# Kernel optimization log

Hardware: AMD Instinct MI355X
Metric: run time of the kernel (lower is better)

Reference implementation:

```python
import jax, jax.numpy as jnp
import numpy as np

B = 1024          # number of graphs
H = 8             # heads
EPS = 1e-5        # LayerNorm eps (torch default)
MEAN_RES_SCALE = 0.2


def _ln(x, w, b):
    mu = x.mean(-1, keepdims=True)
    var = ((x - mu) ** 2).mean(-1, keepdims=True)
    return (x - mu) / jnp.sqrt(var + EPS) * w + b


def setup_inputs() -> dict:
    key = jax.random.key(0)
    ks = jax.random.split(key, 10)
    N, D = 262144, 256
    s = 1.0 / np.sqrt(D)
    return {
        "h": jax.random.normal(ks[0], (N, D), jnp.float32),
        "batch": jnp.sort(jax.random.randint(ks[1], (N,), 0, B)),
        "cdr_mask": jax.random.bernoulli(ks[2], 0.2, (N,)),
        "iface_mask": jax.random.bernoulli(ks[3], 0.2, (N,)),
        "ln_kv_w": jnp.ones((D,), jnp.float32),
        "ln_kv_b": jnp.zeros((D,), jnp.float32),
        "ln_q_w": jnp.ones((D,), jnp.float32),
        "ln_q_b": jnp.zeros((D,), jnp.float32),
        "Wk": jax.random.normal(ks[4], (D, D), jnp.float32) * s,
        "Wv": jax.random.normal(ks[5], (D, D), jnp.float32) * s,
        "Wq": jax.random.normal(ks[6], (D, 2 * D), jnp.float32) * (1.0 / np.sqrt(2 * D)),
        "Wres": jax.random.normal(ks[7], (D, D), jnp.float32) * s,
        "Wout": jax.random.normal(ks[8], (D, D), jnp.float32) * s,
        "cdr_bias": jnp.asarray(0.6, jnp.float32),
        "iface_bias": jnp.asarray(0.8, jnp.float32),
        "logit_scale": jnp.asarray(1.0, jnp.float32),
    }


def reference(h, batch, cdr_mask, iface_mask, ln_kv_w, ln_kv_b, ln_q_w, ln_q_b,
              Wk, Wv, Wq, Wres, Wout, cdr_bias, iface_bias, logit_scale):
    N, D = h.shape
    hd = D // H
    # per-graph mean / max pooling (segment reductions; all segments non-empty)
    counts = jax.ops.segment_sum(jnp.ones((N,), h.dtype), batch, num_segments=B)[:, None]
    mean_raw = jax.ops.segment_sum(h, batch, num_segments=B) / counts      # [B,D]
    max_raw = jax.ops.segment_max(h, batch, num_segments=B)                # [B,D]
    # single query per graph (dropout = identity in eval)
    q = jnp.concatenate([mean_raw, max_raw], axis=-1) @ Wq.T               # [B,D]
    q = _ln(q, ln_q_w, ln_q_b).reshape(B, H, hd)                           # [B,H,hd]
    # keys / values per node
    h_ln = _ln(h, ln_kv_w, ln_kv_b)
    k = (h_ln @ Wk.T).reshape(N, H, hd)
    v = (h_ln @ Wv.T).reshape(N, H, hd)
    # attention logits with mask biases
    logit = (k * q[batch]).sum(-1) * (logit_scale / np.sqrt(hd))           # [N,H]
    logit = logit + cdr_bias * cdr_mask.astype(h.dtype)[:, None]
    logit = logit + iface_bias * iface_mask.astype(h.dtype)[:, None]
    # segment softmax over nodes of each graph
    m = jax.ops.segment_max(logit, batch, num_segments=B)                  # [B,H]
    e = jnp.exp(logit - m[batch])
    z = jax.ops.segment_sum(e, batch, num_segments=B)                      # [B,H]
    attn = e / z[batch]                                                    # [N,H]
    g = jax.ops.segment_sum(attn[..., None] * v, batch, num_segments=B)    # [B,H,hd]
    g = g.reshape(B, D)
    return g @ Wout.T + MEAN_RES_SCALE * (mean_raw @ Wres.T)               # [B,D]
```

## Files before the change

kernel.cpp:

```cpp
#include <hip/hip_runtime.h>

__global__ void k_offsets(const int* __restrict__ batch, int* __restrict__ start,
                          int N, int B) {
    int i = blockIdx.x * blockDim.x + threadIdx.x;
    if (i >= N) return;
    int b = batch[i];
    if (i == 0) {
        for (int g = 0; g <= b; ++g) start[g] = 0;
    } else {
        int pb = batch[i - 1];
        for (int g = pb + 1; g <= b; ++g) start[g] = i;
    }
    if (i == N - 1) {
        for (int g = b + 1; g <= B; ++g) start[g] = N;
    }
}

__global__ __launch_bounds__(256) void k_pool_q(
    const float* __restrict__ h, const int* __restrict__ start,
    const float* __restrict__ Wq, const float* __restrict__ Wk,
    const float* __restrict__ ln_q_w, const float* __restrict__ ln_q_b,
    const float* __restrict__ logit_scale,
    float* __restrict__ mean_raw, float* __restrict__ w_eff)
{
    const int g = blockIdx.x;
    const int d = threadIdx.x;
    const int s = start[g], e = start[g + 1];

    float sum = 0.f, mx = -INFINITY;
    int n = s;
    for (; n + 4 <= e; n += 4) {
        float a0 = h[(size_t)(n + 0) * 256 + d];
        float a1 = h[(size_t)(n + 1) * 256 + d];
        float a2 = h[(size_t)(n + 2) * 256 + d];
        float a3 = h[(size_t)(n + 3) * 256 + d];
        sum += (a0 + a1) + (a2 + a3);
        mx = fmaxf(mx, fmaxf(fmaxf(a0, a1), fmaxf(a2, a3)));
    }
    for (; n < e; ++n) {
        float a = h[(size_t)n * 256 + d];
        sum += a; mx = fmaxf(mx, a);
    }
    const float mean = sum / (float)(e - s);
    mean_raw[(size_t)g * 256 + d] = mean;

    __shared__ float X[512];
    __shared__ float QL[256];
    __shared__ float rs[4], rq[4];
    X[d] = mean;
    X[256 + d] = mx;
    __syncthreads();

    float q = 0.f;
    const float* wqr = Wq + (size_t)d * 512;
    #pragma unroll 8
    for (int j = 0; j < 512; j += 4) {
        float4 w4 = *(const float4*)(wqr + j);
        q += w4.x * X[j] + w4.y * X[j + 1] + w4.z * X[j + 2] + w4.w * X[j + 3];
    }
    float s1 = q, s2 = q * q;
    #pragma unroll
    for (int off = 1; off < 64; off <<= 1) {
        s1 += __shfl_xor(s1, off);
        s2 += __shfl_xor(s2, off);
    }
    if ((d & 63) == 0) { rs[d >> 6] = s1; rq[d >> 6] = s2; }
    __syncthreads();
    const float t1 = rs[0] + rs[1] + rs[2] + rs[3];
    const float t2 = rq[0] + rq[1] + rq[2] + rq[3];
    const float mu = t1 * (1.f / 256.f);
    const float var = t2 * (1.f / 256.f) - mu * mu;
    const float rstd = rsqrtf(var + 1e-5f);
    QL[d] = (q - mu) * rstd * ln_q_w[d] + ln_q_b[d];
    __syncthreads();

    const float scale = logit_scale[0] * 0.17677669529663687f;
    #pragma unroll
    for (int hh = 0; hh < 8; ++hh) {
        float a = 0.f;
        #pragma unroll 8
        for (int r = 0; r < 32; ++r) {
            a += Wk[(size_t)(hh * 32 + r) * 256 + d] * QL[hh * 32 + r];
        }
        w_eff[((size_t)g * 8 + hh) * 256 + d] = a * scale;
    }
}

__global__ __launch_bounds__(256) void k_attn(
    const float* __restrict__ h, const int* __restrict__ start,
    const int* __restrict__ cdr, const int* __restrict__ ifm,
    const float* __restrict__ ln_w, const float* __restrict__ ln_b,
    const float* __restrict__ w_eff,
    const float* __restrict__ cdr_bias, const float* __restrict__ iface_bias,
    float* __restrict__ u_norm)
{
    const int g = blockIdx.x;
    const int tid = threadIdx.x;
    const int w = tid >> 6;
    const int l = tid & 63;
    const int hh = l >> 3;
    const int p = l & 7;
    const int s = start[g], e = start[g + 1];
    const float cb = cdr_bias[0], ib = iface_bias[0];

    const float4 lnw = *(const float4*)(ln_w + l * 4);
    const float4 lnb = *(const float4*)(ln_b + l * 4);

    float we[32];
    {
        const float* wp = w_eff + ((size_t)g * 8 + hh) * 256 + p * 32;
        #pragma unroll
        for (int r = 0; r < 8; ++r) {
            float4 t = *(const float4*)(wp + r * 4);
            we[4 * r + 0] = t.x; we[4 * r + 1] = t.y; we[4 * r + 2] = t.z; we[4 * r + 3] = t.w;
        }
    }

    float m = -INFINITY, z = 0.f;
    float u[32];
    #pragma unroll
    for (int r = 0; r < 32; ++r) u[r] = 0.f;

    __shared__ float hbuf[4][288];
    __shared__ float UF[4][8][256];
    __shared__ float MW[4][8], ZW[4][8], FG[4][8], IZ[8];

    const int wofs = l * 4 + ((l >> 3) << 2);
    const int rofs = p * 36;

    for (int n = s + w; n < e; n += 4) {
        const float4 x = *(const float4*)(h + (size_t)n * 256 + l * 4);
        float s1 = (x.x + x.y) + (x.z + x.w);
        float s2 = x.x * x.x + x.y * x.y + x.z * x.z + x.w * x.w;
        #pragma unroll
        for (int off = 1; off < 64; off <<= 1) {
            s1 += __shfl_xor(s1, off);
            s2 += __shfl_xor(s2, off);
        }
        const float mu = s1 * (1.f / 256.f);
        const float var = s2 * (1.f / 256.f) - mu * mu;
        const float rstd = rsqrtf(var + 1e-5f);
        float4 hl;
        hl.x = (x.x - mu) * rstd * lnw.x + lnb.x;
        hl.y = (x.y - mu) * rstd * lnw.y + lnb.y;
        hl.z = (x.z - mu) * rstd * lnw.z + lnb.z;
        hl.w = (x.w - mu) * rstd * lnw.w + lnb.w;
        *(float4*)(&hbuf[w][wofs]) = hl;
        asm volatile("s_waitcnt lgkmcnt(0)" ::: "memory");

        float hv[32];
        #pragma unroll
        for (int r = 0; r < 8; ++r) {
            float4 t = *(const float4*)(&hbuf[w][rofs + r * 4]);
            hv[4 * r + 0] = t.x; hv[4 * r + 1] = t.y; hv[4 * r + 2] = t.z; hv[4 * r + 3] = t.w;
        }
        float part = 0.f;
        #pragma unroll
        for (int r = 0; r < 32; ++r) part += hv[r] * we[r];
        part += __shfl_xor(part, 1);
        part += __shfl_xor(part, 2);
        part += __shfl_xor(part, 4);

        const float mb = cb * (float)cdr[n] + ib * (float)ifm[n];
        const float lv = part + mb;
        const float nm = fmaxf(m, lv);
        const float a  = __expf(m - nm);
        const float ee = __expf(lv - nm);
        z = z * a + ee;
        #pragma unroll
        for (int r = 0; r < 32; ++r) u[r] = u[r] * a + ee * hv[r];
        m = nm;
    }

    if (p == 0) { MW[w][hh] = m; ZW[w][hh] = z; }
    #pragma unroll
    for (int r = 0; r < 8; ++r) {
        float4 t = make_float4(u[4 * r], u[4 * r + 1], u[4 * r + 2], u[4 * r + 3]);
        *(float4*)(&UF[w][hh][p * 32 + r * 4]) = t;
    }
    __syncthreads();

    if (tid < 8) {
        const float mg = fmaxf(fmaxf(MW[0][tid], MW[1][tid]),
                               fmaxf(MW[2][tid], MW[3][tid]));
        float zg = 0.f;
        #pragma unroll
        for (int ww = 0; ww < 4; ++ww) {
            const float f = __expf(MW[ww][tid] - mg);
            FG[ww][tid] = f;
            zg += ZW[ww][tid] * f;
        }
        IZ[tid] = 1.f / zg;
    }
    __syncthreads();

    #pragma unroll
    for (int it = 0; it < 8; ++it) {
        const int idx = it * 256 + tid;
        const int h2 = idx >> 8, j = idx & 255;
        const float v = UF[0][h2][j] * FG[0][h2] + UF[1][h2][j] * FG[1][h2]
                      + UF[2][h2][j] * FG[2][h2] + UF[3][h2][j] * FG[3][h2];
        u_norm[(size_t)g * 2048 + idx] = v * IZ[h2];
    }
}

__global__ __launch_bounds__(256) void k_out(
    const float* __restrict__ u_norm, const float* __restrict__ mean_raw,
    const float* __restrict__ Wv, const float* __restrict__ Wout,
    const float* __restrict__ Wres, float* __restrict__ out)
{
    const int d = threadIdx.x;
    const int g0 = blockIdx.x * 4;
    __shared__ float UN[4][8][256];
    __shared__ float MR[4][256];
    __shared__ float GF[4][256];

    for (int idx = d; idx < 4 * 2048; idx += 256)
        ((float*)UN)[idx] = u_norm[(size_t)g0 * 2048 + idx];
    for (int idx = d; idx < 4 * 256; idx += 256)
        ((float*)MR)[idx] = mean_raw[(size_t)g0 * 256 + idx];
    __syncthreads();

    const int hh = d >> 5;
    float acc[4] = {0.f, 0.f, 0.f, 0.f};
    const float* wvr = Wv + (size_t)d * 256;
    for (int j = 0; j < 256; j += 4) {
        const float4 wv = *(const float4*)(wvr + j);
        #pragma unroll
        for (int gg = 0; gg < 4; ++gg) {
            acc[gg] += wv.x * UN[gg][hh][j]     + wv.y * UN[gg][hh][j + 1]
                     + wv.z * UN[gg][hh][j + 2] + wv.w * UN[gg][hh][j + 3];
        }
    }
    #pragma unroll
    for (int gg = 0; gg < 4; ++gg) GF[gg][d] = acc[gg];
    __syncthreads();

    float oo[4] = {0.f, 0.f, 0.f, 0.f};
    float rr[4] = {0.f, 0.f, 0.f, 0.f};
    const float* wor = Wout + (size_t)d * 256;
    const float* wrr = Wres + (size_t)d * 256;
    for (int j = 0; j < 256; j += 4) {
        const float4 wo = *(const float4*)(wor + j);
        const float4 wq = *(const float4*)(wrr + j);
        #pragma unroll
        for (int gg = 0; gg < 4; ++gg) {
            oo[gg] += wo.x * GF[gg][j]     + wo.y * GF[gg][j + 1]
                    + wo.z * GF[gg][j + 2] + wo.w * GF[gg][j + 3];
            rr[gg] += wq.x * MR[gg][j]     + wq.y * MR[gg][j + 1]
                    + wq.z * MR[gg][j + 2] + wq.w * MR[gg][j + 3];
        }
    }
    #pragma unroll
    for (int gg = 0; gg < 4; ++gg)
        out[(size_t)(g0 + gg) * 256 + d] = oo[gg] + 0.2f * rr[gg];
}

extern "C" void kernel_launch(void* const* d_in, const int* in_sizes, int n_in,
                              void* d_out, int out_size, void* d_ws, size_t ws_size,
                              hipStream_t stream)
{
    const float* h        = (const float*)d_in[0];
    const int*   batch    = (const int*)d_in[1];
    const int*   cdr      = (const int*)d_in[2];
    const int*   ifm      = (const int*)d_in[3];
    const float* ln_kv_w  = (const float*)d_in[4];
    const float* ln_kv_b  = (const float*)d_in[5];
    const float* ln_q_w   = (const float*)d_in[6];
    const float* ln_q_b   = (const float*)d_in[7];
    const float* Wk       = (const float*)d_in[8];
    const float* Wv       = (const float*)d_in[9];
    const float* Wq       = (const float*)d_in[10];
    const float* Wres     = (const float*)d_in[11];
    const float* Wout     = (const float*)d_in[12];
    const float* cdr_b    = (const float*)d_in[13];
    const float* if_b     = (const float*)d_in[14];
    const float* lsc      = (const float*)d_in[15];

    const int N = in_sizes[0] / 256;
    const int B = out_size / 256;

    int*   start    = (int*)d_ws;
    float* mean_raw = (float*)((char*)d_ws + 8192);
    float* w_eff    = mean_raw + (size_t)B * 256;
    float* u_norm   = w_eff + (size_t)B * 2048;

    k_offsets<<<(N + 255) / 256, 256, 0, stream>>>(batch, start, N, B);
    k_pool_q<<<B, 256, 0, stream>>>(h, start, Wq, Wk, ln_q_w, ln_q_b, lsc,
                                    mean_raw, w_eff);
    k_attn<<<B, 256, 0, stream>>>(h, start, cdr, ifm, ln_kv_w, ln_kv_b, w_eff,
                                  cdr_b, if_b, u_norm);
    k_out<<<B / 4, 256, 0, stream>>>(u_norm, mean_raw, Wv, Wout, Wres, (float*)d_out);
}
```

Measured before the change: 666.5 us.

## Fold LayerNorm into attention weights, prefetch nodes, vectorize pooling, regrid output kernel

The kv LayerNorm is folded algebraically. The ln weight goes into w_eff, and the logit is computed as rstd*(h·w - mu*sum(w)). The weighted sums use raw h with a separate mean correction, and the affine is applied once per graph at the end, which removes the 6-step per-node wave reduction and the normalize pass. The attention loop also prefetches the next node, skips the rescale when no lane's max increases, and pads the shared UF array. Pooling now reads float4 with four waves splitting the nodes, and k_out runs one graph per block instead of four. Computing on raw rather than normalized values can change floating-point accuracy.

```diff
diff --git a/kernel.cpp b/kernel.cpp
--- a/kernel.cpp
+++ b/kernel.cpp
@@ -20,35 +20,48 @@
     const float* __restrict__ h, const int* __restrict__ start,
     const float* __restrict__ Wq, const float* __restrict__ Wk,
     const float* __restrict__ ln_q_w, const float* __restrict__ ln_q_b,
-    const float* __restrict__ logit_scale,
+    const float* __restrict__ ln_kv_w, const float* __restrict__ logit_scale,
     float* __restrict__ mean_raw, float* __restrict__ w_eff)
 {
     const int g = blockIdx.x;
-    const int d = threadIdx.x;
+    const int tid = threadIdx.x;
+    const int w = tid >> 6;
+    const int l = tid & 63;
+    const int d = tid;
     const int s = start[g], e = start[g + 1];
 
-    float sum = 0.f, mx = -INFINITY;
-    int n = s;
-    for (; n + 4 <= e; n += 4) {
-        float a0 = h[(size_t)(n + 0) * 256 + d];
-        float a1 = h[(size_t)(n + 1) * 256 + d];
-        float a2 = h[(size_t)(n + 2) * 256 + d];
-        float a3 = h[(size_t)(n + 3) * 256 + d];
-        sum += (a0 + a1) + (a2 + a3);
-        mx = fmaxf(mx, fmaxf(fmaxf(a0, a1), fmaxf(a2, a3)));
-    }
-    for (; n < e; ++n) {
-        float a = h[(size_t)n * 256 + d];
-        sum += a; mx = fmaxf(mx, a);
-    }
+    float4 sm = make_float4(0.f, 0.f, 0.f, 0.f);
+    float4 mx = make_float4(-INFINITY, -INFINITY, -INFINITY, -INFINITY);
+    int n = s + w;
+    for (; n + 4 < e; n += 8) {
+        const float4 a = *(const float4*)(h + (size_t)n * 256 + l * 4);
+        const float4 b = *(const float4*)(h + (size_t)(n + 4) * 256 + l * 4);
+        sm.x += a.x + b.x; sm.y += a.y + b.y; sm.z += a.z + b.z; sm.w += a.w + b.w;
+        mx.x = fmaxf(mx.x, fmaxf(a.x, b.x)); mx.y = fmaxf(mx.y, fmaxf(a.y, b.y));
+        mx.z = fmaxf(mx.z, fmaxf(a.z, b.z)); mx.w = fmaxf(mx.w, fmaxf(a.w, b.w));
+    }
+    if (n < e) {
+        const float4 a = *(const float4*)(h + (size_t)n * 256 + l * 4);
+        sm.x += a.x; sm.y += a.y; sm.z += a.z; sm.w += a.w;
+        mx.x = fmaxf(mx.x, a.x); mx.y = fmaxf(mx.y, a.y);
+        mx.z = fmaxf(mx.z, a.z); mx.w = fmaxf(mx.w, a.w);
+    }
+
+    __shared__ __align__(16) float PS[4][256];
+    __shared__ __align__(16) float PM[4][256];
+    *(float4*)(&PS[w][l * 4]) = sm;
+    *(float4*)(&PM[w][l * 4]) = mx;
+    __syncthreads();
+    const float sum = (PS[0][d] + PS[1][d]) + (PS[2][d] + PS[3][d]);
+    const float mxv = fmaxf(fmaxf(PM[0][d], PM[1][d]), fmaxf(PM[2][d], PM[3][d]));
     const float mean = sum / (float)(e - s);
     mean_raw[(size_t)g * 256 + d] = mean;
 
-    __shared__ float X[512];
+    __shared__ __align__(16) float X[512];
     __shared__ float QL[256];
     __shared__ float rs[4], rq[4];
     X[d] = mean;
-    X[256 + d] = mx;
+    X[256 + d] = mxv;
     __syncthreads();
 
     float q = 0.f;
@@ -75,6 +88,7 @@
     __syncthreads();
 
     const float scale = logit_scale[0] * 0.17677669529663687f;
+    const float fold = scale * ln_kv_w[d];
     #pragma unroll
     for (int hh = 0; hh < 8; ++hh) {
         float a = 0.f;
@@ -82,11 +96,11 @@
         for (int r = 0; r < 32; ++r) {
             a += Wk[(size_t)(hh * 32 + r) * 256 + d] * QL[hh * 32 + r];
         }
-        w_eff[((size_t)g * 8 + hh) * 256 + d] = a * scale;
-    }
-}
-
-__global__ __launch_bounds__(256) void k_attn(
+        w_eff[((size_t)g * 8 + hh) * 256 + d] = a * fold;
+    }
+}
+
+__global__ __launch_bounds__(256, 4) void k_attn(
     const float* __restrict__ h, const int* __restrict__ start,
     const int* __restrict__ cdr, const int* __restrict__ ifm,
     const float* __restrict__ ln_w, const float* __restrict__ ln_b,
@@ -103,9 +117,6 @@
     const int s = start[g], e = start[g + 1];
     const float cb = cdr_bias[0], ib = iface_bias[0];
 
-    const float4 lnw = *(const float4*)(ln_w + l * 4);
-    const float4 lnb = *(const float4*)(ln_b + l * 4);
-
     float we[32];
     {
         const float* wp = w_eff + ((size_t)g * 8 + hh) * 256 + p * 32;
@@ -115,64 +126,90 @@
             we[4 * r + 0] = t.x; we[4 * r + 1] = t.y; we[4 * r + 2] = t.z; we[4 * r + 3] = t.w;
         }
     }
-
-    float m = -INFINITY, z = 0.f;
+    float s1h = 0.f;
+    #pragma unroll
+    for (int r = 0; r < 32; ++r) s1h += we[r];
+    s1h += __shfl_xor(s1h, 1);
+    s1h += __shfl_xor(s1h, 2);
+    s1h += __shfl_xor(s1h, 4);
+
+    float m = -INFINITY, z = 0.f, sw = 0.f;
     float u[32];
     #pragma unroll
     for (int r = 0; r < 32; ++r) u[r] = 0.f;
 
-    __shared__ float hbuf[4][288];
-    __shared__ float UF[4][8][256];
-    __shared__ float MW[4][8], ZW[4][8], FG[4][8], IZ[8];
+    __shared__ __align__(16) float hbuf[4][288];
+    __shared__ __align__(16) float UF[4][8][264];
+    __shared__ float MW[4][8], ZW[4][8], SW[4][8], FG[4][8], IZ[8], SG[8];
 
     const int wofs = l * 4 + ((l >> 3) << 2);
     const int rofs = p * 36;
 
-    for (int n = s + w; n < e; n += 4) {
-        const float4 x = *(const float4*)(h + (size_t)n * 256 + l * 4);
-        float s1 = (x.x + x.y) + (x.z + x.w);
-        float s2 = x.x * x.x + x.y * x.y + x.z * x.z + x.w * x.w;
-        #pragma unroll
-        for (int off = 1; off < 64; off <<= 1) {
+    int n = s + w;
+    float4 xn = make_float4(0.f, 0.f, 0.f, 0.f);
+    int cn = 0, im = 0;
+    if (n < e) {
+        xn = *(const float4*)(h + (size_t)n * 256 + l * 4);
+        cn = cdr[n]; im = ifm[n];
+    }
+    while (n < e) {
+        const float4 xc = xn;
+        const int cc = cn, ic = im;
+        const int n2 = n + 4;
+        if (n2 < e) {
+            xn = *(const float4*)(h + (size_t)n2 * 256 + l * 4);
+            cn = cdr[n2]; im = ifm[n2];
+        }
+
+        *(float4*)(&hbuf[w][wofs]) = xc;
+        asm volatile("s_waitcnt lgkmcnt(0)" ::: "memory");
+
+        float hv[32];
+        #pragma unroll
+        for (int r = 0; r < 8; ++r) {
+            float4 t = *(const float4*)(&hbuf[w][rofs + r * 4]);
+            hv[4 * r + 0] = t.x; hv[4 * r + 1] = t.y; hv[4 * r + 2] = t.z; hv[4 * r + 3] = t.w;
+        }
+        float s1 = 0.f, s2 = 0.f, dt = 0.f;
+        #pragma unroll
+        for (int r = 0; r < 32; ++r) {
+            const float v = hv[r];
+            s1 += v;
+            s2 = fmaf(v, v, s2);
+            dt = fmaf(v, we[r], dt);
+        }
+        #pragma unroll
+        for (int off = 1; off < 8; off <<= 1) {
             s1 += __shfl_xor(s1, off);
             s2 += __shfl_xor(s2, off);
+            dt += __shfl_xor(dt, off);
         }
         const float mu = s1 * (1.f / 256.f);
         const float var = s2 * (1.f / 256.f) - mu * mu;
         const float rstd = rsqrtf(var + 1e-5f);
-        float4 hl;
-        hl.x = (x.x - mu) * rstd * lnw.x + lnb.x;
-        hl.y = (x.y - mu) * rstd * lnw.y + lnb.y;
-        hl.z = (x.z - mu) * rstd * lnw.z + lnb.z;
-        hl.w = (x.w - mu) * rstd * lnw.w + lnb.w;
-        *(float4*)(&hbuf[w][wofs]) = hl;
-        asm volatile("s_waitcnt lgkmcnt(0)" ::: "memory");
-
-        float hv[32];
-        #pragma unroll
-        for (int r = 0; r < 8; ++r) {
-            float4 t = *(const float4*)(&hbuf[w][rofs + r * 4]);
-            hv[4 * r + 0] = t.x; hv[4 * r + 1] = t.y; hv[4 * r + 2] = t.z; hv[4 * r + 3] = t.w;
-        }
-        float part = 0.f;
-        #pragma unroll
-        for (int r = 0; r < 32; ++r) part += hv[r] * we[r];
-        part += __shfl_xor(part, 1);
-        part += __shfl_xor(part, 2);
-        part += __shfl_xor(part, 4);
-
-        const float mb = cb * (float)cdr[n] + ib * (float)ifm[n];
-        const float lv = part + mb;
+        const float mb = cb * (float)cc + ib * (float)ic;
+        const float lv = rstd * (dt - mu * s1h) + mb;
+
         const float nm = fmaxf(m, lv);
-        const float a  = __expf(m - nm);
         const float ee = __expf(lv - nm);
-        z = z * a + ee;
-        #pragma unroll
-        for (int r = 0; r < 32; ++r) u[r] = u[r] * a + ee * hv[r];
-        m = nm;
-    }
-
-    if (p == 0) { MW[w][hh] = m; ZW[w][hh] = z; }
+        const float c = ee * rstd;
+        if (__any(lv > m)) {
+            const float a = __expf(m - nm);
+            z = z * a + ee;
+            sw = sw * a + c * mu;
+            #pragma unroll
+            for (int r = 0; r < 32; ++r) u[r] = u[r] * a + c * hv[r];
+            m = nm;
+        } else {
+            z += ee;
+            sw += c * mu;
+            #pragma unroll
+            for (int r = 0; r < 32; ++r) u[r] = fmaf(c, hv[r], u[r]);
+        }
+        n = n2;
+    }
+
+    if (p == 0) { MW[w][hh] = m; ZW[w][hh] = z; SW[w][hh] = sw; }
     #pragma unroll
     for (int r = 0; r < 8; ++r) {
         float4 t = make_float4(u[4 * r], u[4 * r + 1], u[4 * r + 2], u[4 * r + 3]);
@@ -183,24 +220,25 @@
     if (tid < 8) {
         const float mg = fmaxf(fmaxf(MW[0][tid], MW[1][tid]),
                                fmaxf(MW[2][tid], MW[3][tid]));
-        float zg = 0.f;
+        float zg = 0.f, sg = 0.f;
         #pragma unroll
         for (int ww = 0; ww < 4; ++ww) {
             const float f = __expf(MW[ww][tid] - mg);
             FG[ww][tid] = f;
             zg += ZW[ww][tid] * f;
+            sg += SW[ww][tid] * f;
         }
         IZ[tid] = 1.f / zg;
-    }
-    __syncthreads();
-
-    #pragma unroll
-    for (int it = 0; it < 8; ++it) {
-        const int idx = it * 256 + tid;
-        const int h2 = idx >> 8, j = idx & 255;
-        const float v = UF[0][h2][j] * FG[0][h2] + UF[1][h2][j] * FG[1][h2]
-                      + UF[2][h2][j] * FG[2][h2] + UF[3][h2][j] * FG[3][h2];
-        u_norm[(size_t)g * 2048 + idx] = v * IZ[h2];
+        SG[tid] = sg;
+    }
+    __syncthreads();
+
+    const float lwj = ln_w[tid], lbj = ln_b[tid];
+    #pragma unroll
+    for (int h2 = 0; h2 < 8; ++h2) {
+        const float Uv = UF[0][h2][tid] * FG[0][h2] + UF[1][h2][tid] * FG[1][h2]
+                       + UF[2][h2][tid] * FG[2][h2] + UF[3][h2][tid] * FG[3][h2];
+        u_norm[(size_t)g * 2048 + h2 * 256 + tid] = (Uv - SG[h2]) * IZ[h2] * lwj + lbj;
     }
 }
 
@@ -210,50 +248,42 @@
     const float* __restrict__ Wres, float* __restrict__ out)
 {
     const int d = threadIdx.x;
-    const int g0 = blockIdx.x * 4;
-    __shared__ float UN[4][8][256];
-    __shared__ float MR[4][256];
-    __shared__ float GF[4][256];
-
-    for (int idx = d; idx < 4 * 2048; idx += 256)
-        ((float*)UN)[idx] = u_norm[(size_t)g0 * 2048 + idx];
-    for (int idx = d; idx < 4 * 256; idx += 256)
-        ((float*)MR)[idx] = mean_raw[(size_t)g0 * 256 + idx];
+    const int g = blockIdx.x;
+    __shared__ __align__(16) float UN[8][256];
+    __shared__ __align__(16) float MR[256];
+    __shared__ __align__(16) float GF[256];
+
+    const float4* up = (const float4*)(u_norm + (size_t)g * 2048);
+    ((float4*)UN)[d] = up[d];
+    ((float4*)UN)[256 + d] = up[256 + d];
+    if (d < 64) ((float4*)MR)[d] = ((const float4*)(mean_raw + (size_t)g * 256))[d];
     __syncthreads();
 
     const int hh = d >> 5;
-    float acc[4] = {0.f, 0.f, 0.f, 0.f};
+    float acc = 0.f;
     const float* wvr = Wv + (size_t)d * 256;
+    #pragma unroll 8
     for (int j = 0; j < 256; j += 4) {
         const float4 wv = *(const float4*)(wvr + j);
-        #pragma unroll
-        for (int gg = 0; gg < 4; ++gg) {
-            acc[gg] += wv.x * UN[gg][hh][j]     + wv.y * UN[gg][hh][j + 1]
-                     + wv.z * UN[gg][hh][j + 2] + wv.w * UN[gg][hh][j + 3];
-        }
-    }
-    #pragma unroll
-    for (int gg = 0; gg < 4; ++gg) GF[gg][d] = acc[gg];
-    __syncthreads();
-
-    float oo[4] = {0.f, 0.f, 0.f, 0.f};
-    float rr[4] = {0.f, 0.f, 0.f, 0.f};
+        const float4 uv = *(const float4*)(&UN[hh][j]);
+        acc += wv.x * uv.x + wv.y * uv.y + wv.z * uv.z + wv.w * uv.w;
+    }
+    GF[d] = acc;
+    __syncthreads();
+
+    float oo = 0.f, rr = 0.f;
     const float* wor = Wout + (size_t)d * 256;
     const float* wrr = Wres + (size_t)d * 256;
+    #pragma unroll 8
     for (int j = 0; j < 256; j += 4) {
         const float4 wo = *(const float4*)(wor + j);
         const float4 wq = *(const float4*)(wrr + j);
-        #pragma unroll
-        for (int gg = 0; gg < 4; ++gg) {
-            oo[gg] += wo.x * GF[gg][j]     + wo.y * GF[gg][j + 1]
-                    + wo.z * GF[gg][j + 2] + wo.w * GF[gg][j + 3];
-            rr[gg] += wq.x * MR[gg][j]     + wq.y * MR[gg][j + 1]
-                    + wq.z * MR[gg][j + 2] + wq.w * MR[gg][j + 3];
-        }
-    }
-    #pragma unroll
-    for (int gg = 0; gg < 4; ++gg)
-        out[(size_t)(g0 + gg) * 256 + d] = oo[gg] + 0.2f * rr[gg];
+        const float4 gf = *(const float4*)(&GF[j]);
+        const float4 mr = *(const float4*)(&MR[j]);
+        oo += wo.x * gf.x + wo.y * gf.y + wo.z * gf.z + wo.w * gf.w;
+        rr += wq.x * mr.x + wq.y * mr.y + wq.z * mr.z + wq.w * mr.w;
+    }
+    out[(size_t)g * 256 + d] = oo + 0.2f * rr;
 }
 
 extern "C" void kernel_launch(void* const* d_in, const int* in_sizes, int n_in,
@@ -286,9 +316,9 @@
     float* u_norm   = w_eff + (size_t)B * 2048;
 
     k_offsets<<<(N + 255) / 256, 256, 0, stream>>>(batch, start, N, B);
-    k_pool_q<<<B, 256, 0, stream>>>(h, start, Wq, Wk, ln_q_w, ln_q_b, lsc,
+    k_pool_q<<<B, 256, 0, stream>>>(h, start, Wq, Wk, ln_q_w, ln_q_b, ln_kv_w, lsc,
                                     mean_raw, w_eff);
     k_attn<<<B, 256, 0, stream>>>(h, start, cdr, ifm, ln_kv_w, ln_kv_b, w_eff,
                                   cdr_b, if_b, u_norm);
-    k_out<<<B / 4, 256, 0, stream>>>(u_norm, mean_raw, Wv, Wout, Wres, (float*)d_out);
-}
+    k_out<<<B, 256, 0, stream>>>(u_norm, mean_raw, Wv, Wout, Wres, (float*)d_out);
+}
```

Result: slower. 949.8 us (+42.5%).
